# Kernel optimization log

Measured on AMD Instinct MI355X. Metric: run time of the kernel, lower is better.

## Reference

```python
import jax, jax.numpy as jnp
import numpy as np

NUM_HEADS = 8
DIM = 256
SCALE = (DIM // NUM_HEADS) ** -0.5  # head_dim = dim // nhead = 32


def setup_inputs() -> dict:
    key = jax.random.key(0)
    k1, k2, k3, k4, k5 = jax.random.split(key, 5)
    B, N = 1, 4096
    qk = jax.random.normal(k1, (B, N, 3 * DIM), dtype=jnp.float32)
    v_cls = jax.random.normal(k2, (B, N, 2 * DIM), dtype=jnp.float32)
    masks = jax.random.uniform(k3, (B, N, N), dtype=jnp.float32)
    # torch Linear weights stored as [in, out] for x @ W
    W_qk = jax.random.normal(k4, (3 * DIM, 6 * DIM), dtype=jnp.float32) * (3 * DIM) ** -0.5
    W_v = jax.random.normal(k5, (2 * DIM, 2 * DIM), dtype=jnp.float32) * (2 * DIM) ** -0.5
    return {"qk": qk, "v_cls": v_cls, "masks": masks, "W_qk": W_qk, "W_v": W_v}


def reference(qk, v_cls, masks, W_qk, W_v):
    B, N, C_qk = qk.shape
    C_cls = v_cls.shape[-1]
    H = NUM_HEADS
    hd_qk = C_qk // H   # 96
    hd_v = C_cls // H   # 64

    # qk projection: [B,N,6*dim] -> (2,B,H,N,hd_qk)
    proj = (qk @ W_qk).reshape(B, N, 2, H, hd_qk).transpose(2, 0, 3, 1, 4)
    q, k = proj[0], proj[1]                      # [B,H,N,hd_qk]
    v = (v_cls @ W_v).reshape(B, N, H, hd_v).transpose(0, 2, 1, 3)  # [B,H,N,hd_v]

    attn = jnp.einsum('bhnd,bhmd->bhnm', q, k) * SCALE
    attn = jax.nn.softmax(attn, axis=-1)

    # post-softmax mask-mul and renorm by mask-sum and head count
    m = masks[:, None]                           # [B,1,N,N] broadcast over heads
    attn = attn * m / (H * jnp.sum(m, axis=-1, keepdims=True))
    # attn_drop with p=0.0 is identity in eval

    x_cls = jnp.einsum('bhnm,bhmd->bhnd', attn, v)
    return x_cls.transpose(0, 2, 1, 3).reshape(B, N, C_cls)
```

## Files before the change

kernel.cpp:

```cpp
#include <hip/hip_runtime.h>

typedef __attribute__((ext_vector_type(8))) _Float16 half8;
typedef __attribute__((ext_vector_type(4))) _Float16 half4;
typedef __attribute__((ext_vector_type(2))) _Float16 half2;
typedef __attribute__((ext_vector_type(2))) __fp16 fp16x2;
typedef __attribute__((ext_vector_type(4))) float f32x4;

#define N_SEQ 4096
#define HD_QK 96
#define HD_V  64
#define NHEADS 8
#define QSCALE 0.25505545556f
#define ESHIFT 8.0f

union PKC { fp16x2 p; half2 h; };

__device__ inline half2 pk_cvt(float a, float b) {
    PKC u;
    u.p = __builtin_amdgcn_cvt_pkrtz(a, b);
    return u.h;
}

__device__ inline half8 cvt8(float4 a, float4 b) {
    half8 h;
    h[0] = (_Float16)a.x; h[1] = (_Float16)a.y; h[2] = (_Float16)a.z; h[3] = (_Float16)a.w;
    h[4] = (_Float16)b.x; h[5] = (_Float16)b.y; h[6] = (_Float16)b.z; h[7] = (_Float16)b.w;
    return h;
}

__device__ inline void cast_blk(const float* __restrict__ in, _Float16* __restrict__ out,
                                int blk, int t) {
    size_t i = ((size_t)blk * 256 + t) * 8;
    float4 a = *(const float4*)(in + i);
    float4 b = *(const float4*)(in + i + 4);
    *(half8*)(out + i) = cvt8(a, b);
}

__device__ __forceinline__ void gl16(const void* g, void* l) {
    __builtin_amdgcn_global_load_lds(
        (const __attribute__((address_space(1))) unsigned int*)g,
        (__attribute__((address_space(3))) unsigned int*)l, 16, 0, 0);
}

__global__ __launch_bounds__(256) void prep(
    const float* __restrict__ qk, const float* __restrict__ v_cls,
    const float* __restrict__ masks, const float* __restrict__ W_qk,
    const float* __restrict__ W_v,
    _Float16* __restrict__ Xh, _Float16* __restrict__ Vch,
    _Float16* __restrict__ Msw, float* __restrict__ Msum,
    _Float16* __restrict__ Wqkt, _Float16* __restrict__ Wvt)
{
    __shared__ float tile[32][33];
    __shared__ float red[64][17];
    const int bx = blockIdx.x, t = threadIdx.x;
    if (bx < 1536) {
        cast_blk(qk, Xh, bx, t);
    } else if (bx < 2560) {
        cast_blk(v_cls, Vch, bx - 1536, t);
    } else if (bx < 3968) {
        const bool big = bx < 3712;
        const int id = big ? bx - 2560 : bx - 3712;
        const int nx = big ? 48 : 16;
        const int C = big ? 1536 : 512, R = big ? 768 : 512;
        const float* in = big ? W_qk : W_v;
        _Float16* out = big ? Wqkt : Wvt;
        int cx = id % nx, cy = id / nx;
        int tx = t & 31, ty = t >> 5;
        int c0 = cx * 32, r0 = cy * 32;
        for (int k = 0; k < 4; k++)
            tile[ty + 8 * k][tx] = in[(size_t)(r0 + ty + 8 * k) * C + c0 + tx];
        __syncthreads();
        for (int k = 0; k < 4; k++)
            out[(size_t)(c0 + ty + 8 * k) * R + r0 + tx] = (_Float16)tile[tx][ty + 8 * k];
    } else {
        const int id = bx - 3968;
        const int q0b = id >> 6, kb = id & 63;
        const int w = t >> 6, lane = t & 63;
        const int l15 = lane >> 2, quad = lane & 3;
        const int col = kb * 64 + 16 * w + 4 * quad;
        half4 hv[4];
        float ps[4];
        for (int nt = 0; nt < 4; nt++) {
            const float* src = masks + (size_t)(q0b * 64 + 16 * nt + l15) * N_SEQ + col;
            float4 a = *(const float4*)src;
            hv[nt] = half4{(_Float16)a.x, (_Float16)a.y, (_Float16)a.z, (_Float16)a.w};
            ps[nt] = (a.x + a.y) + (a.z + a.w);
        }
        _Float16* dst = Msw + (((size_t)(q0b * 64 + kb) * 4 + w) * 1024) + lane * 16;
        half8 h0, h1;
        for (int j = 0; j < 4; j++) {
            h0[j] = hv[0][j]; h0[4 + j] = hv[1][j];
            h1[j] = hv[2][j]; h1[4 + j] = hv[3][j];
        }
        *(half8*)dst = h0;
        *(half8*)(dst + 8) = h1;
        for (int nt = 0; nt < 4; nt++)
            red[16 * nt + l15][w * 4 + quad] = ps[nt];
        __syncthreads();
        if (t < 64) {
            float s = 0.f;
            for (int i = 0; i < 16; i++) s += red[t][i];
            atomicAdd(&Msum[q0b * 64 + t], s);
        }
    }
}

__global__ __launch_bounds__(256) void proj_fused(
    const _Float16* __restrict__ Xh, const _Float16* __restrict__ Vch,
    const _Float16* __restrict__ Wqkt, const _Float16* __restrict__ Wvt,
    _Float16* __restrict__ Qh, _Float16* __restrict__ Kh,
    _Float16* __restrict__ Vtg)
{
    __shared__ _Float16 smem[192 * 72];
    _Float16 (*Xs)[72] = (_Float16 (*)[72])smem;
    _Float16 (*Ws)[72] = (_Float16 (*)[72])(smem + 128 * 72);

    const int t = threadIdx.x;
    const int lane = t & 63, wv = t >> 6;
    const int quad = lane >> 4, l15 = lane & 15;
    const bool qkmode = blockIdx.x < 24;
    const int n0 = qkmode ? blockIdx.x * 64 : (blockIdx.x - 24) * 64;
    const int row0 = blockIdx.y * 128;
    const int K = qkmode ? 768 : 512;
    const _Float16* X = qkmode ? Xh : Vch;
    const _Float16* Wt = qkmode ? Wqkt : Wvt;

    const int mB = (wv & 1) * 64, nB = (wv >> 1) * 32;
    const int sr = t >> 1, sk = (t & 1) * 32;
    const int sr2 = t >> 2, sk2 = (t & 3) * 16;

    const f32x4 fzero = {0.f, 0.f, 0.f, 0.f};
    f32x4 acc[4][2];
    for (int i = 0; i < 4; i++)
        for (int j = 0; j < 2; j++) acc[i][j] = fzero;

    for (int k0 = 0; k0 < K; k0 += 64) {
        __syncthreads();
        {
            const _Float16* xp = X + (size_t)(row0 + sr) * K + k0 + sk;
            *(half8*)&Xs[sr][sk]      = *(const half8*)xp;
            *(half8*)&Xs[sr][sk + 8]  = *(const half8*)(xp + 8);
            *(half8*)&Xs[sr][sk + 16] = *(const half8*)(xp + 16);
            *(half8*)&Xs[sr][sk + 24] = *(const half8*)(xp + 24);
            const _Float16* wp = Wt + (size_t)(n0 + sr2) * K + k0 + sk2;
            *(half8*)&Ws[sr2][sk2]     = *(const half8*)wp;
            *(half8*)&Ws[sr2][sk2 + 8] = *(const half8*)(wp + 8);
        }
        __syncthreads();
        for (int c = 0; c < 2; c++) {
            half8 af[4], bf[2];
            for (int i = 0; i < 4; i++)
                af[i] = *(const half8*)&Xs[mB + 16 * i + l15][c * 32 + quad * 8];
            for (int j = 0; j < 2; j++)
                bf[j] = *(const half8*)&Ws[nB + 16 * j + l15][c * 32 + quad * 8];
            for (int i = 0; i < 4; i++)
                for (int j = 0; j < 2; j++)
                    acc[i][j] = __builtin_amdgcn_mfma_f32_16x16x32_f16(af[i], bf[j], acc[i][j], 0, 0, 0);
        }
    }

    __syncthreads();
    _Float16 (*Ct)[72] = (_Float16 (*)[72])smem;
    for (int j = 0; j < 2; j++) {
        int col = n0 + nB + 16 * j + l15;
        float scl = (qkmode && col < 768) ? QSCALE : 1.0f;
        for (int i = 0; i < 4; i++)
            for (int r = 0; r < 4; r++)
                Ct[mB + 16 * i + quad * 4 + r][nB + 16 * j + l15] =
                    (_Float16)(acc[i][j][r] * scl);
    }
    __syncthreads();

    if (qkmode) {
        for (int e = 0; e < 4; e++) {
            int id = e * 256 + t;
            int row = id >> 3, cc = id & 7;
            int col = n0 + cc * 8;
            int w = col >= 768 ? 1 : 0;
            int rem = col - w * 768;
            int h = rem / 96, d = rem - h * 96;
            _Float16* dst = w ? Kh : Qh;
            *(half8*)&dst[((size_t)h * N_SEQ + row0 + row) * HD_QK + d] =
                *(const half8*)&Ct[row][cc * 8];
        }
    } else {
        for (int e = 0; e < 2; e++) {
            int id = e * 256 + t;
            int col = id >> 3, rc = id & 7;
            int c = n0 + col;
            int h = c >> 6, d = c & 63;
            half8 v0, v1;
            for (int k = 0; k < 8; k++) {
                v0[k] = Ct[rc * 16 + k][col];
                v1[k] = Ct[rc * 16 + 8 + k][col];
            }
            _Float16* dst = &Vtg[((size_t)h * HD_V + d) * N_SEQ + row0 + rc * 16];
            *(half8*)dst = v0;
            *(half8*)(dst + 8) = v1;
        }
    }
}

__global__ __launch_bounds__(256, 3) void flash_attn(
    const _Float16* __restrict__ Qh, const _Float16* __restrict__ Kh,
    const _Float16* __restrict__ Vtg, const _Float16* __restrict__ Msw,
    _Float16* __restrict__ Owsh, float* __restrict__ Lws)
{
    __shared__ __align__(16) char smem[40960];

    const int t = threadIdx.x;
    const int lane = t & 63, w = t >> 6;
    const int quad = lane >> 4, l15 = lane & 15;
    const int bx = blockIdx.x;
    const int q0b = bx & 63;
    const int hz = bx >> 6;
    const int head = hz & 7;
    const int z = hz >> 3;
    const int q0 = q0b * 64;
    const int kb0 = 21 * z, kbE = (z == 2) ? 64 : kb0 + 21;

    half8 qf[3][4];
    for (int nt = 0; nt < 4; nt++) {
        const _Float16* qp = Qh + ((size_t)head * N_SEQ + q0 + 16 * nt + l15) * HD_QK + 8 * quad;
        for (int c = 0; c < 3; c++)
            qf[c][nt] = *(const half8*)(qp + 32 * c);
    }

    const char* kgb = (const char*)Kh
        + ((size_t)(head * N_SEQ + 16 * w + l15) * HD_QK + 8 * quad) * 2;
    const char* vgb = (const char*)Vtg
        + ((size_t)(head * HD_V + lane) * N_SEQ) * 2 + 32 * w;
    const _Float16* mbase = Msw + ((size_t)(q0b * 64 + kb0) * 4 + w) * 1024
                                + (l15 * 4 + quad) * 16;

    char* stW = smem + w * 10240;

    const f32x4 fzero = {0.f, 0.f, 0.f, 0.f};
    const f32x4 minit = {-ESHIFT, -ESHIFT, -ESHIFT, -ESHIFT};
    f32x4 oacc[4][4];
    for (int nt = 0; nt < 4; nt++)
        for (int v = 0; v < 4; v++) oacc[nt][v] = fzero;
    float lsum[4] = {0.f, 0.f, 0.f, 0.f};

    half8 m01, m23;

    {
        char* kd = stW;
        const char* ks = kgb + (size_t)kb0 * 12288;
        gl16(ks, kd);
        gl16(ks + 64, kd + 1024);
        gl16(ks + 128, kd + 2048);
        char* vd = stW + 3072;
        const char* vs = vgb + (size_t)kb0 * 128;
        gl16(vs, vd);
        gl16(vs + 16, vd + 1024);
    }
    m01 = *(const half8*)mbase;
    m23 = *(const half8*)(mbase + 8);

    int cur = 0;
    for (int j = kb0; j < kbE; j++, cur ^= 1) {
        asm volatile("s_waitcnt vmcnt(2)" ::: "memory");
        __builtin_amdgcn_sched_barrier(0);

        const char* kl = stW + cur * 5120;
        half8 kf[3];
        kf[0] = *(const half8*)(kl + lane * 16);
        kf[1] = *(const half8*)(kl + 1024 + lane * 16);
        kf[2] = *(const half8*)(kl + 2048 + lane * 16);
        const char* vl = kl + 3072 + (quad >> 1) * 1024 + l15 * 16 + (quad & 1) * 8;
        half4 vf[4];
        vf[0] = *(const half4*)(vl);
        vf[1] = *(const half4*)(vl + 256);
        vf[2] = *(const half4*)(vl + 512);
        vf[3] = *(const half4*)(vl + 768);

        const int jn = (j + 1 < kbE) ? j + 1 : j;
        {
            char* kd = stW + (cur ^ 1) * 5120;
            const char* ks = kgb + (size_t)jn * 12288;
            gl16(ks, kd);
            gl16(ks + 64, kd + 1024);
            gl16(ks + 128, kd + 2048);
            char* vd = kd + 3072;
            const char* vs = vgb + (size_t)jn * 128;
            gl16(vs, vd);
            gl16(vs + 16, vd + 1024);
        }

        f32x4 sT[4];
        for (int nt = 0; nt < 4; nt++) {
            f32x4 s = __builtin_amdgcn_mfma_f32_16x16x32_f16(kf[0], qf[0][nt], minit, 0, 0, 0);
            s = __builtin_amdgcn_mfma_f32_16x16x32_f16(kf[1], qf[1][nt], s, 0, 0, 0);
            s = __builtin_amdgcn_mfma_f32_16x16x32_f16(kf[2], qf[2][nt], s, 0, 0, 0);
            sT[nt] = s;
        }

        half4 af[4];
        {
            half2 mh[8];
            for (int i = 0; i < 4; i++) {
                mh[i]     = half2{m01[2 * i], m01[2 * i + 1]};
                mh[4 + i] = half2{m23[2 * i], m23[2 * i + 1]};
            }
            for (int nt = 0; nt < 4; nt++) {
                float p0 = exp2f(sT[nt][0]);
                float p1 = exp2f(sT[nt][1]);
                float p2 = exp2f(sT[nt][2]);
                float p3 = exp2f(sT[nt][3]);
                lsum[nt] += (p0 + p1) + (p2 + p3);
                half2 lo = pk_cvt(p0, p1) * mh[2 * nt];
                half2 hi = pk_cvt(p2, p3) * mh[2 * nt + 1];
                af[nt] = half4{lo[0], lo[1], hi[0], hi[1]};
            }
        }
        {
            const _Float16* mp = mbase + (size_t)(jn - kb0) * 4096;
            m01 = *(const half8*)mp;
            m23 = *(const half8*)(mp + 8);
        }

        for (int nt = 0; nt < 4; nt++)
            for (int v = 0; v < 4; v++)
                oacc[nt][v] = __builtin_amdgcn_mfma_f32_16x16x16f16(af[nt], vf[v], oacc[nt][v], 0, 0, 0);
    }

    __syncthreads();

    float (*Ob)[64][68] = (float (*)[64][68])smem;
    float (*Lb)[64] = (float (*)[64])(smem + 34816);

    for (int nt = 0; nt < 4; nt++) {
        lsum[nt] += __shfl_xor(lsum[nt], 16);
        lsum[nt] += __shfl_xor(lsum[nt], 32);
    }

    if (w & 1) {
        for (int nt = 0; nt < 4; nt++) {
            for (int v = 0; v < 4; v++)
                for (int r = 0; r < 4; r++)
                    Ob[w >> 1][16 * nt + 4 * quad + r][16 * v + l15] = oacc[nt][v][r];
            if (quad == 0) Lb[w >> 1][16 * nt + l15] = lsum[nt];
        }
    }
    __syncthreads();
    if (!(w & 1)) {
        for (int nt = 0; nt < 4; nt++) {
            for (int v = 0; v < 4; v++)
                for (int r = 0; r < 4; r++)
                    Ob[w >> 1][16 * nt + 4 * quad + r][16 * v + l15] += oacc[nt][v][r];
            if (quad == 0) Lb[w >> 1][16 * nt + l15] += lsum[nt];
        }
    }
    __syncthreads();

    {
        int row = t >> 2, c0 = (t & 3) * 16;
        _Float16* obase = Owsh + (size_t)z * N_SEQ * 512 + (size_t)(q0 + row) * 512
                          + head * HD_V + c0;
        for (int g = 0; g < 2; g++) {
            half8 h;
            for (int j2 = 0; j2 < 8; j2++)
                h[j2] = (_Float16)(Ob[0][row][c0 + 8 * g + j2] + Ob[1][row][c0 + 8 * g + j2]);
            *(half8*)(obase + 8 * g) = h;
        }
        if (t < 64)
            Lws[((size_t)z * NHEADS + head) * N_SEQ + q0 + t] = Lb[0][t] + Lb[1][t];
    }
}

__global__ __launch_bounds__(256) void finalize(
    const _Float16* __restrict__ Owsh, const float* __restrict__ Lws,
    const float* __restrict__ Msum, float* __restrict__ out)
{
    const size_t ZSTR = (size_t)N_SEQ * 512;
    size_t o = ((size_t)blockIdx.x * 256 + threadIdx.x) * 8;
    int q = (int)(o >> 9);
    int head = (int)((o & 511) >> 6);
    half8 p0 = *(const half8*)(Owsh + o);
    half8 p1 = *(const half8*)(Owsh + ZSTR + o);
    half8 p2 = *(const half8*)(Owsh + 2 * ZSTR + o);
    float l = Lws[(size_t)head * N_SEQ + q]
            + Lws[((size_t)NHEADS + head) * N_SEQ + q]
            + Lws[((size_t)2 * NHEADS + head) * N_SEQ + q];
    float inv = 1.0f / (l * (float)NHEADS * Msum[q]);
    float4 r0, r1;
    r0.x = ((float)p0[0] + (float)p1[0] + (float)p2[0]) * inv;
    r0.y = ((float)p0[1] + (float)p1[1] + (float)p2[1]) * inv;
    r0.z = ((float)p0[2] + (float)p1[2] + (float)p2[2]) * inv;
    r0.w = ((float)p0[3] + (float)p1[3] + (float)p2[3]) * inv;
    r1.x = ((float)p0[4] + (float)p1[4] + (float)p2[4]) * inv;
    r1.y = ((float)p0[5] + (float)p1[5] + (float)p2[5]) * inv;
    r1.z = ((float)p0[6] + (float)p1[6] + (float)p2[6]) * inv;
    r1.w = ((float)p0[7] + (float)p1[7] + (float)p2[7]) * inv;
    *(float4*)(out + o) = r0;
    *(float4*)(out + o + 4) = r1;
}

extern "C" void kernel_launch(void* const* d_in, const int* in_sizes, int n_in,
                              void* d_out, int out_size, void* d_ws, size_t ws_size,
                              hipStream_t stream) {
    const float* qk    = (const float*)d_in[0];
    const float* v_cls = (const float*)d_in[1];
    const float* masks = (const float*)d_in[2];
    const float* W_qk  = (const float*)d_in[3];
    const float* W_v   = (const float*)d_in[4];
    float* out = (float*)d_out;

    char* wsp = (char*)d_ws;
    _Float16* Xh   = (_Float16*)(wsp);
    _Float16* Vch  = (_Float16*)(wsp + (size_t)6291456);
    _Float16* Wqkt = (_Float16*)(wsp + (size_t)10485760);
    _Float16* Wvt  = (_Float16*)(wsp + (size_t)12845056);
    _Float16* Owsh = (_Float16*)(wsp);
    size_t off = 13631488;
    auto allocB = [&](size_t bytes) { char* p = wsp + off; off += (bytes + 255) & ~(size_t)255; return p; };
    _Float16* Qh   = (_Float16*)allocB((size_t)NHEADS * N_SEQ * HD_QK * 2);
    _Float16* Kh   = (_Float16*)allocB((size_t)NHEADS * N_SEQ * HD_QK * 2);
    _Float16* Vtg  = (_Float16*)allocB((size_t)NHEADS * HD_V * N_SEQ * 2);
    _Float16* Msw  = (_Float16*)allocB((size_t)N_SEQ * N_SEQ * 2);
    float*    Msum = (float*)allocB((size_t)N_SEQ * 4);
    float*    Lws  = (float*)allocB((size_t)3 * NHEADS * N_SEQ * 4);
    (void)ws_size;

    dim3 blk(256);
    (void)hipMemsetAsync(Msum, 0, N_SEQ * sizeof(float), stream);
    prep<<<dim3(8064), blk, 0, stream>>>(
        qk, v_cls, masks, W_qk, W_v, Xh, Vch, Msw, Msum, Wqkt, Wvt);

    proj_fused<<<dim3(32, N_SEQ / 128), blk, 0, stream>>>(
        Xh, Vch, Wqkt, Wvt, Qh, Kh, Vtg);

    flash_attn<<<dim3(1536), blk, 0, stream>>>(
        Qh, Kh, Vtg, Msw, Owsh, Lws);

    finalize<<<dim3((N_SEQ * 512) / (256 * 8)), blk, 0, stream>>>(
        Owsh, Lws, Msum, out);
}
```

Before: 267.3 us.

## Load K fragments directly to registers with two-step-ahead prefetch, shrink LDS staging

K fragments are now loaded straight from global memory into registers two iterations ahead, in two ping-pong register sets with a 2x-unrolled loop. Only V is staged through LDS, so per-wave LDS drops from 10KB to 4KB. The attention loop uses hardware exp2 intrinsics and sched_barriers to pin the order of loads and MFMAs. Prefetching past the end is covered by padding the workspace with an extra allocation. This raises register pressure and relies on manual vmcnt accounting, with the aim of cutting LDS round trips and load latency.

```diff
diff --git a/kernel.cpp b/kernel.cpp
--- a/kernel.cpp
+++ b/kernel.cpp
@@ -201,12 +201,77 @@
     }
 }
 
+#define FA_STEP(KF, SLOT, J)                                                  \
+    do {                                                                      \
+        asm volatile("s_waitcnt vmcnt(5)" ::: "memory");                      \
+        __builtin_amdgcn_sched_barrier(0);                                    \
+        const char* vl_ = stW + (SLOT) * 2048 + (quad >> 1) * 1024            \
+                          + l15 * 16 + (quad & 1) * 8;                        \
+        half4 vf0 = *(const half4*)(vl_);                                     \
+        half4 vf1 = *(const half4*)(vl_ + 256);                               \
+        half4 vf2 = *(const half4*)(vl_ + 512);                               \
+        half4 vf3 = *(const half4*)(vl_ + 768);                               \
+        __builtin_amdgcn_sched_barrier(0);                                    \
+        {                                                                     \
+            const char* vs_ = vgb + (size_t)((J) + 1) * 128;                  \
+            char* vd_ = stW + (1 - (SLOT)) * 2048;                            \
+            gl16(vs_, vd_);                                                   \
+            gl16(vs_ + 16, vd_ + 1024);                                       \
+        }                                                                     \
+        __builtin_amdgcn_sched_barrier(0);                                    \
+        f32x4 sT[4];                                                          \
+        for (int nt = 0; nt < 4; nt++) {                                      \
+            f32x4 s = __builtin_amdgcn_mfma_f32_16x16x32_f16(KF[0], qf[0][nt], minit, 0, 0, 0); \
+            s = __builtin_amdgcn_mfma_f32_16x16x32_f16(KF[1], qf[1][nt], s, 0, 0, 0); \
+            s = __builtin_amdgcn_mfma_f32_16x16x32_f16(KF[2], qf[2][nt], s, 0, 0, 0); \
+            sT[nt] = s;                                                       \
+        }                                                                     \
+        half4 af[4];                                                          \
+        {                                                                     \
+            half2 mh[8];                                                      \
+            for (int i = 0; i < 4; i++) {                                     \
+                mh[i]     = half2{m01[2 * i], m01[2 * i + 1]};                \
+                mh[4 + i] = half2{m23[2 * i], m23[2 * i + 1]};                \
+            }                                                                 \
+            for (int nt = 0; nt < 4; nt++) {                                  \
+                float p0 = __builtin_amdgcn_exp2f(sT[nt][0]);                 \
+                float p1 = __builtin_amdgcn_exp2f(sT[nt][1]);                 \
+                float p2 = __builtin_amdgcn_exp2f(sT[nt][2]);                 \
+                float p3 = __builtin_amdgcn_exp2f(sT[nt][3]);                 \
+                lsum[nt] += (p0 + p1) + (p2 + p3);                            \
+                half2 lo = pk_cvt(p0, p1) * mh[2 * nt];                       \
+                half2 hi = pk_cvt(p2, p3) * mh[2 * nt + 1];                   \
+                af[nt] = half4{lo[0], lo[1], hi[0], hi[1]};                   \
+            }                                                                 \
+        }                                                                     \
+        __builtin_amdgcn_sched_barrier(0);                                    \
+        {                                                                     \
+            const _Float16* mp_ = mbase + (size_t)((J) + 1 - kb0) * 4096;     \
+            m01 = *(const half8*)mp_;                                         \
+            m23 = *(const half8*)(mp_ + 8);                                   \
+        }                                                                     \
+        __builtin_amdgcn_sched_barrier(0);                                    \
+        {                                                                     \
+            const char* kp_ = kgb + (size_t)((J) + 2) * 12288;                \
+            KF[0] = *(const half8*)(kp_);                                     \
+            KF[1] = *(const half8*)(kp_ + 64);                                \
+            KF[2] = *(const half8*)(kp_ + 128);                               \
+        }                                                                     \
+        __builtin_amdgcn_sched_barrier(0);                                    \
+        for (int nt = 0; nt < 4; nt++) {                                      \
+            oacc[nt][0] = __builtin_amdgcn_mfma_f32_16x16x16f16(af[nt], vf0, oacc[nt][0], 0, 0, 0); \
+            oacc[nt][1] = __builtin_amdgcn_mfma_f32_16x16x16f16(af[nt], vf1, oacc[nt][1], 0, 0, 0); \
+            oacc[nt][2] = __builtin_amdgcn_mfma_f32_16x16x16f16(af[nt], vf2, oacc[nt][2], 0, 0, 0); \
+            oacc[nt][3] = __builtin_amdgcn_mfma_f32_16x16x16f16(af[nt], vf3, oacc[nt][3], 0, 0, 0); \
+        }                                                                     \
+    } while (0)
+
 __global__ __launch_bounds__(256, 3) void flash_attn(
     const _Float16* __restrict__ Qh, const _Float16* __restrict__ Kh,
     const _Float16* __restrict__ Vtg, const _Float16* __restrict__ Msw,
     _Float16* __restrict__ Owsh, float* __restrict__ Lws)
 {
-    __shared__ __align__(16) char smem[40960];
+    __shared__ __align__(16) char smem[35328];
 
     const int t = threadIdx.x;
     const int lane = t & 63, w = t >> 6;
@@ -233,7 +298,7 @@
     const _Float16* mbase = Msw + ((size_t)(q0b * 64 + kb0) * 4 + w) * 1024
                                 + (l15 * 4 + quad) * 16;
 
-    char* stW = smem + w * 10240;
+    char* stW = smem + w * 4096;
 
     const f32x4 fzero = {0.f, 0.f, 0.f, 0.f};
     const f32x4 minit = {-ESHIFT, -ESHIFT, -ESHIFT, -ESHIFT};
@@ -242,87 +307,40 @@
         for (int v = 0; v < 4; v++) oacc[nt][v] = fzero;
     float lsum[4] = {0.f, 0.f, 0.f, 0.f};
 
+    half8 kfA[3], kfB[3];
     half8 m01, m23;
 
     {
-        char* kd = stW;
-        const char* ks = kgb + (size_t)kb0 * 12288;
-        gl16(ks, kd);
-        gl16(ks + 64, kd + 1024);
-        gl16(ks + 128, kd + 2048);
-        char* vd = stW + 3072;
+        const char* kp = kgb + (size_t)kb0 * 12288;
+        kfA[0] = *(const half8*)(kp);
+        kfA[1] = *(const half8*)(kp + 64);
+        kfA[2] = *(const half8*)(kp + 128);
+    }
+    __builtin_amdgcn_sched_barrier(0);
+    {
         const char* vs = vgb + (size_t)kb0 * 128;
-        gl16(vs, vd);
-        gl16(vs + 16, vd + 1024);
-    }
+        gl16(vs, stW);
+        gl16(vs + 16, stW + 1024);
+    }
+    __builtin_amdgcn_sched_barrier(0);
     m01 = *(const half8*)mbase;
     m23 = *(const half8*)(mbase + 8);
-
-    int cur = 0;
-    for (int j = kb0; j < kbE; j++, cur ^= 1) {
-        asm volatile("s_waitcnt vmcnt(2)" ::: "memory");
-        __builtin_amdgcn_sched_barrier(0);
-
-        const char* kl = stW + cur * 5120;
-        half8 kf[3];
-        kf[0] = *(const half8*)(kl + lane * 16);
-        kf[1] = *(const half8*)(kl + 1024 + lane * 16);
-        kf[2] = *(const half8*)(kl + 2048 + lane * 16);
-        const char* vl = kl + 3072 + (quad >> 1) * 1024 + l15 * 16 + (quad & 1) * 8;
-        half4 vf[4];
-        vf[0] = *(const half4*)(vl);
-        vf[1] = *(const half4*)(vl + 256);
-        vf[2] = *(const half4*)(vl + 512);
-        vf[3] = *(const half4*)(vl + 768);
-
-        const int jn = (j + 1 < kbE) ? j + 1 : j;
-        {
-            char* kd = stW + (cur ^ 1) * 5120;
-            const char* ks = kgb + (size_t)jn * 12288;
-            gl16(ks, kd);
-            gl16(ks + 64, kd + 1024);
-            gl16(ks + 128, kd + 2048);
-            char* vd = kd + 3072;
-            const char* vs = vgb + (size_t)jn * 128;
-            gl16(vs, vd);
-            gl16(vs + 16, vd + 1024);
-        }
-
-        f32x4 sT[4];
-        for (int nt = 0; nt < 4; nt++) {
-            f32x4 s = __builtin_amdgcn_mfma_f32_16x16x32_f16(kf[0], qf[0][nt], minit, 0, 0, 0);
-            s = __builtin_amdgcn_mfma_f32_16x16x32_f16(kf[1], qf[1][nt], s, 0, 0, 0);
-            s = __builtin_amdgcn_mfma_f32_16x16x32_f16(kf[2], qf[2][nt], s, 0, 0, 0);
-            sT[nt] = s;
-        }
-
-        half4 af[4];
-        {
-            half2 mh[8];
-            for (int i = 0; i < 4; i++) {
-                mh[i]     = half2{m01[2 * i], m01[2 * i + 1]};
-                mh[4 + i] = half2{m23[2 * i], m23[2 * i + 1]};
-            }
-            for (int nt = 0; nt < 4; nt++) {
-                float p0 = exp2f(sT[nt][0]);
-                float p1 = exp2f(sT[nt][1]);
-                float p2 = exp2f(sT[nt][2]);
-                float p3 = exp2f(sT[nt][3]);
-                lsum[nt] += (p0 + p1) + (p2 + p3);
-                half2 lo = pk_cvt(p0, p1) * mh[2 * nt];
-                half2 hi = pk_cvt(p2, p3) * mh[2 * nt + 1];
-                af[nt] = half4{lo[0], lo[1], hi[0], hi[1]};
-            }
-        }
-        {
-            const _Float16* mp = mbase + (size_t)(jn - kb0) * 4096;
-            m01 = *(const half8*)mp;
-            m23 = *(const half8*)(mp + 8);
-        }
-
-        for (int nt = 0; nt < 4; nt++)
-            for (int v = 0; v < 4; v++)
-                oacc[nt][v] = __builtin_amdgcn_mfma_f32_16x16x16f16(af[nt], vf[v], oacc[nt][v], 0, 0, 0);
+    __builtin_amdgcn_sched_barrier(0);
+    {
+        const char* kp = kgb + (size_t)(kb0 + 1) * 12288;
+        kfB[0] = *(const half8*)(kp);
+        kfB[1] = *(const half8*)(kp + 64);
+        kfB[2] = *(const half8*)(kp + 128);
+    }
+    __builtin_amdgcn_sched_barrier(0);
+
+    int j = kb0;
+    for (; j + 1 < kbE; j += 2) {
+        FA_STEP(kfA, 0, j);
+        FA_STEP(kfB, 1, j + 1);
+    }
+    if (j < kbE) {
+        FA_STEP(kfA, 0, j);
     }
 
     __syncthreads();
@@ -368,6 +386,8 @@
             Lws[((size_t)z * NHEADS + head) * N_SEQ + q0 + t] = Lb[0][t] + Lb[1][t];
     }
 }
+
+#undef FA_STEP
 
 __global__ __launch_bounds__(256) void finalize(
     const _Float16* __restrict__ Owsh, const float* __restrict__ Lws,
@@ -421,6 +441,7 @@
     _Float16* Msw  = (_Float16*)allocB((size_t)N_SEQ * N_SEQ * 2);
     float*    Msum = (float*)allocB((size_t)N_SEQ * 4);
     float*    Lws  = (float*)allocB((size_t)3 * NHEADS * N_SEQ * 4);
+    (void)allocB((size_t)131072);
     (void)ws_size;
 
     dim3 blk(256);
```

Measured after the change: 569.9 us. 2.13x slower.
